# Performance work log

Hardware: AMD Instinct MI355X
Metric: run time of the kernel (lower is better)

## Reference

```python
import jax, jax.numpy as jnp
import numpy as np

GAMMA_LL = 1.7595e11            # gyromagnetic ratio (rad/s/T), class constant
MU0 = np.float32(4e-7 * np.pi)  # vacuum permeability
A_EXCH = 3.65e-12               # exchange stiffness (J/m)
ALPHA = 0.01                    # Gilbert damping (run)
ALPHA_RELAX = 0.5               # high damping used by relax()
DT = 5e-12                      # timestep (s)
DX = DY = 50e-9                 # cell size (m)
NX = NY = 256
T = 1024
RELAX_STEPS = 100               # relax_timesteps class constant


def _laplacian(m):
    # m: (1,3,NX,NY); 5-point Laplacian with Neumann (replicate) boundaries
    mp = jnp.pad(m, ((0, 0), (0, 0), (1, 1), (1, 1)), mode="edge")
    lap_x = (mp[:, :, 2:, 1:-1] + mp[:, :, :-2, 1:-1] - 2.0 * m) / (DX * DX)
    lap_y = (mp[:, :, 1:-1, 2:] + mp[:, :, 1:-1, :-2] - 2.0 * m) / (DY * DY)
    return lap_x + lap_y


def _B_eff(m, B_ext, Msat):
    # B_ext + exchange + (local thin-film) demag
    B_exch = (2.0 * A_EXCH / Msat) * _laplacian(m)
    zhat = jnp.array([0.0, 0.0, 1.0], m.dtype).reshape(1, 3, 1, 1)
    B_demag = -MU0 * Msat * m * zhat
    return B_ext + B_exch + B_demag


def _torque_LLG(m, B_ext, Msat, alpha):
    m_x_B = jnp.cross(m, _B_eff(m, B_ext, Msat), axis=1)
    return -(m_x_B + alpha * jnp.cross(m, m_x_B, axis=1)) / (1.0 + alpha * alpha)


def _rk4_step(m, B_ext, Msat, alpha):
    h = GAMMA_LL * DT
    k1 = _torque_LLG(m, B_ext, Msat, alpha)
    k2 = _torque_LLG(m + 0.5 * h * k1, B_ext, Msat, alpha)
    k3 = _torque_LLG(m + 0.5 * h * k2, B_ext, Msat, alpha)
    k4 = _torque_LLG(m + h * k3, B_ext, Msat, alpha)
    return m + (h / 6.0) * (k1 + 2.0 * k2 + 2.0 * k3 + k4)


def setup_inputs() -> dict:
    key = jax.random.key(0)
    signal = jax.random.normal(key, (1, T, 1), jnp.float32)
    # 60 mT out-of-plane bias field
    B_ext = jnp.zeros((1, 3, NX, NY), jnp.float32).at[:, 2].set(0.06)
    Msat = 1.4e5 * jnp.ones((1, 1, NX, NY), jnp.float32)
    # source antenna: 1 mT/unit signal on Bx in a 20x20 patch
    src_mask = jnp.zeros((1, 3, NX, NY), jnp.float32).at[:, 0, 20:40, 118:138].set(1e-3)
    probe_mask = jnp.zeros((NX, NY), jnp.float32).at[216:236, 118:138].set(1.0)
    return {"signal": signal, "B_ext": B_ext, "Msat": Msat,
            "src_mask": src_mask, "probe_mask": probe_mask}


def reference(signal, B_ext, Msat, src_mask, probe_mask):
    dtype = signal.dtype
    m_init = jnp.zeros((1, 3, NX, NY), dtype).at[:, 2].set(1.0)

    # relax(): high-damping RK4 steps under no_grad
    B_ext_c = jax.lax.stop_gradient(B_ext)
    Msat_c = jax.lax.stop_gradient(Msat)
    m0 = jax.lax.fori_loop(
        0, RELAX_STEPS,
        lambda i, m: _rk4_step(m, B_ext_c, Msat_c, ALPHA_RELAX),
        m_init)
    m0 = jax.lax.stop_gradient(m0)

    pm_sum = jnp.sum(probe_mask)

    def step(m, s):
        Bt = B_ext + s * src_mask            # inject_sources
        m = _rk4_step(m, Bt, Msat, ALPHA)    # rk4_step_LLG
        # measure_probes: mean mx of (m - m0) * Msat over probe region
        out = jnp.sum(((m - m0) * Msat)[:, 0] * probe_mask) / pm_sum
        return m, out

    m_final, outs = jax.lax.scan(jax.checkpoint(step), m0, signal[0, :, 0])
    return outs[None, :]  # (1, T) concatenated probe outputs
```

## Files before the change

### kernel.cpp

```cpp
#include <hip/hip_runtime.h>

#define TST   1024
#define OWN   16
#define HALO  4
#define TDIM  24
#define NT    576
#define NB    256

typedef float v4f __attribute__((ext_vector_type(4)));

#define AG __HIP_MEMORY_SCOPE_AGENT
__device__ __forceinline__ float agload (const float* p){ return __hip_atomic_load (p, __ATOMIC_RELAXED, AG); }
__device__ __forceinline__ int   agloadi(const int* p)  { return __hip_atomic_load (p, __ATOMIC_RELAXED, AG); }
__device__ __forceinline__ void  agstoref(float* p,float v){      __hip_atomic_store(p, v, __ATOMIC_RELAXED, AG); }
__device__ __forceinline__ void  agstorei(int* p,int v) {         __hip_atomic_store(p, v, __ATOMIC_RELAXED, AG); }

__device__ __forceinline__ v4f ld16_dev(const v4f* p) {
    v4f r;
    asm volatile("global_load_dwordx4 %0, %1, off sc1\n\ts_waitcnt vmcnt(0)"
                 : "=v"(r) : "v"(p) : "memory");
    return r;
}
__device__ __forceinline__ void st16_dev(v4f* p, v4f v) {
    asm volatile("global_store_dwordx4 %0, %1, off sc1" :: "v"(p), "v"(v) : "memory");
}

__global__ void __launch_bounds__(NT)
mm_solver(const float* __restrict__ signal,
          const float* __restrict__ B_ext,
          const float* __restrict__ Msat,
          const float* __restrict__ src_mask,
          const float* __restrict__ probe_mask,
          float* __restrict__ out,
          float* __restrict__ ws)
{
    const int b  = (int)blockIdx.x;
    const int bx = b & 15, by = b >> 4;
    const int t  = (int)threadIdx.x;
    const int tr = t / TDIM, tc = t % TDIM;

    const int grow = by * OWN - HALO + tr;
    const int gcol = bx * OWN - HALO + tc;
    const bool inG = (grow >= 0 && grow < 256 && gcol >= 0 && gcol < 256);
    const bool own = (tr >= HALO && tr < HALO + OWN && tc >= HALO && tc < HALO + OWN);

    v4f*   pub   = (v4f*)ws;
    float* priv  = ws + 2 * NB * 256 * 4;
    int*   doneA = (int*)(priv + NB * TST);
    const int pubStride = NB * 256;

    __shared__ v4f  EB[2][TDIM * TDIM];
    __shared__ float sigS[TST];
    __shared__ int   hasP;
    __shared__ int   pfl[NB];
    __shared__ float redS[16];
    __shared__ float pmsS;

    const float invd   = (float)(1.0 / (double)((float)(50e-9 * 50e-9)));
    const float h      = (float)(1.7595e11 * 5e-12);
    const float hh     = (float)(0.5 * (1.7595e11 * 5e-12));
    const float h6     = (float)((1.7595e11 * 5e-12) / 6.0);
    const float alpha  = 0.01f;
    const float inv1a2 = (float)(1.0 / (1.0 + 0.01 * 0.01));

    const int growc = grow < 0 ? 0 : (grow > 255 ? 255 : grow);
    const int gcolc = gcol < 0 ? 0 : (gcol > 255 ? 255 : gcol);
    const int idxg  = growc * 256 + gcolc;
    const float bxv = B_ext[idxg], byv = B_ext[65536 + idxg], bzv = B_ext[131072 + idxg];
    const float ms  = Msat[idxg];
    const float sxv = src_mask[idxg], syv = src_mask[65536 + idxg], szv = src_mask[131072 + idxg];
    const float pm  = probe_mask[idxg];
    const float ce   = 7.3e-12f / ms;
    const float cdem = -(float)(4.0e-7 * 3.14159265358979323846) * ms;

    const int idx  = t;
    const int offU = ((tr < TDIM - 1) && (grow < 255)) ?  TDIM : 0;
    const int offD = ((tr > 0)        && (grow > 0))   ? -TDIM : 0;
    const int offR = ((tc < TDIM - 1) && (gcol < 255)) ?  1 : 0;
    const int offL = ((tc > 0)        && (gcol > 0))   ? -1 : 0;

    const int ownerB  = ((grow >> 4) << 4) | (gcol >> 4);
    const int ownerCi = ((grow & 15) << 4) | (gcol & 15);
    const int slotOff = ownerB * 256 + ownerCi;

    float mx = 0.0f, my = 0.0f, mz = 1.0f;

    if (own) st16_dev(pub + slotOff, (v4f){0.0f, 0.0f, 1.0f, __int_as_float(0)});
    for (int k = t; k < TST; k += NT) sigS[k] = signal[k];
    if (t == 0) hasP = 0;
    __syncthreads();
    const bool pcell = own && (pm != 0.0f);
    if (pcell) atomicOr(&hasP, 1);
    const bool waveP = (__ballot(pcell) != 0ull);
    __syncthreads();
    const int hasPr = hasP;
    if (hasPr) for (int k = t; k < TST; k += NT) agstoref(&priv[b * TST + k], 0.0f);

    const bool haloT = inG && !own;
    float ex, ey, ez, ax, ay, az, kx, ky, kz, btx, bty, btz;

#define STAGE(SB) do { \
    const v4f u = EB[SB][idx + offU]; \
    const v4f d = EB[SB][idx + offD]; \
    const v4f r = EB[SB][idx + offR]; \
    const v4f l = EB[SB][idx + offL]; \
    float lx = ((u.x + d.x - 2.0f * ex) + (r.x + l.x - 2.0f * ex)) * invd; \
    float ly = ((u.y + d.y - 2.0f * ey) + (r.y + l.y - 2.0f * ey)) * invd; \
    float lz = ((u.z + d.z - 2.0f * ez) + (r.z + l.z - 2.0f * ez)) * invd; \
    float Bx = btx + ce * lx; \
    float By = bty + ce * ly; \
    float Bz = btz + ce * lz + cdem * ez; \
    float cx = ey * Bz - ez * By; \
    float cy = ez * Bx - ex * Bz; \
    float cz = ex * By - ey * Bx; \
    float dx = ey * cz - ez * cy; \
    float dy = ez * cx - ex * cz; \
    float dz = ex * cy - ey * cx; \
    kx = -(cx + alpha * dx) * inv1a2; \
    ky = -(cy + alpha * dy) * inv1a2; \
    kz = -(cz + alpha * dz) * inv1a2; \
} while (0)

#define WRE(DB) do { EB[DB][idx] = (v4f){ex, ey, ez, 0.0f}; } while (0)

    for (int i = 0; i < TST; ++i) {
        const float s = sigS[i];

        if (haloT) {
            const v4f* p = pub + (i & 1) * pubStride + slotOff;
            for (;;) {
                v4f hv = ld16_dev(p);
                if (__float_as_int(hv.w) >= i) { mx = hv.x; my = hv.y; mz = hv.z; break; }
                __builtin_amdgcn_s_sleep(1);
            }
        }

        btx = bxv + s * sxv;  bty = byv + s * syv;  btz = bzv + s * szv;
        ex = mx; ey = my; ez = mz;
        WRE(0);
        __syncthreads();

        STAGE(0);
        ax = kx; ay = ky; az = kz;
        ex = mx + hh * kx; ey = my + hh * ky; ez = mz + hh * kz;
        WRE(1);
        __syncthreads();

        STAGE(1);
        ax += 2.0f * kx; ay += 2.0f * ky; az += 2.0f * kz;
        ex = mx + hh * kx; ey = my + hh * ky; ez = mz + hh * kz;
        WRE(0);
        __syncthreads();

        STAGE(0);
        ax += 2.0f * kx; ay += 2.0f * ky; az += 2.0f * kz;
        ex = mx + h * kx; ey = my + h * ky; ez = mz + h * kz;
        WRE(1);
        __syncthreads();

        STAGE(1);
        ax += kx; ay += ky; az += kz;
        mx += h6 * ax; my += h6 * ay; mz += h6 * az;

        if (own) st16_dev(pub + ((i + 1) & 1) * pubStride + slotOff,
                          (v4f){mx, my, mz, __int_as_float(i + 1)});

        if (waveP) {
            float c = pcell ? mx * ms * pm : 0.0f;
            #pragma unroll
            for (int off = 32; off > 0; off >>= 1) c += __shfl_down(c, off, 64);
            if ((t & 63) == 0) atomicAdd(&priv[b * TST + i], c);
        }
    }

    __syncthreads();
    if (t == 0) agstorei(&doneA[b], 0x5D0000 | hasPr);

    if (b == 0) {
        if (t < NB) {
            int v;
            for (;;) { v = agloadi(&doneA[t]); if ((v & ~1) == 0x5D0000) break;
                       __builtin_amdgcn_s_sleep(8); }
            pfl[t] = v & 1;
        }
        __syncthreads();
        float ps = 0.0f;
        for (int k = t; k < 65536; k += NT) ps += probe_mask[k];
        #pragma unroll
        for (int off = 32; off > 0; off >>= 1) ps += __shfl_down(ps, off, 64);
        if ((t & 63) == 0) redS[t >> 6] = ps;
        __syncthreads();
        if (t == 0) { float q = 0.0f; for (int w = 0; w < 9; ++w) q += redS[w]; pmsS = q; }
        __syncthreads();
        const float pms = pmsS;
        for (int o = t; o < TST; o += NT) {
            float sm = 0.0f;
            for (int j = 0; j < NB; ++j) if (pfl[j]) sm += agload(&priv[j * TST + o]);
            out[o] = sm / pms;
        }
    }
}

extern "C" void kernel_launch(void* const* d_in, const int* in_sizes, int n_in,
                              void* d_out, int out_size, void* d_ws, size_t ws_size,
                              hipStream_t stream)
{
    const float* signal = (const float*)d_in[0];
    const float* B_ext  = (const float*)d_in[1];
    const float* Msat   = (const float*)d_in[2];
    const float* src    = (const float*)d_in[3];
    const float* probe  = (const float*)d_in[4];
    float* out = (float*)d_out;
    float* ws  = (float*)d_ws;

    void* args[] = { &signal, &B_ext, &Msat, &src, &probe, &out, &ws };
    (void)in_sizes; (void)n_in; (void)out_size; (void)ws_size;

    hipLaunchCooperativeKernel(reinterpret_cast<void*>(mm_solver),
                               dim3(NB), dim3(NT), args, 0, stream);
}
```

Baseline: 3.217 ms.

## Replace block barriers with per-wave neighbor counters in LDS

Each of the four `__syncthreads` per RK4 step is replaced by point-to-point sync. Every wave publishes a stage counter in shared memory and spins only until its two adjacent waves have reached the same stage, which the 5-point stencil needs. The s_sleep in the halo polling loop is also removed. The global exchange buffer is re-indexed in plain row-major cell order instead of owner-block order. The intent is to cut barrier latency and wakeup delay, at the cost of busy-spinning on LDS and relying on subtle ordering (WAR hazards between the double buffers) for correctness.

New measurement: 2.985 ms. 1.08x faster.

```diff
diff --git a/kernel.cpp b/kernel.cpp
--- a/kernel.cpp
+++ b/kernel.cpp
@@ -38,6 +38,7 @@
     const int bx = b & 15, by = b >> 4;
     const int t  = (int)threadIdx.x;
     const int tr = t / TDIM, tc = t % TDIM;
+    const int wv = t >> 6;
 
     const int grow = by * OWN - HALO + tr;
     const int gcol = bx * OWN - HALO + tc;
@@ -45,16 +46,33 @@
     const bool own = (tr >= HALO && tr < HALO + OWN && tc >= HALO && tc < HALO + OWN);
 
     v4f*   pub   = (v4f*)ws;
-    float* priv  = ws + 2 * NB * 256 * 4;
+    float* priv  = ws + 2 * 65536 * 4;
     int*   doneA = (int*)(priv + NB * TST);
-    const int pubStride = NB * 256;
+    const int pubStride = 65536;
 
     __shared__ v4f  EB[2][TDIM * TDIM];
     __shared__ float sigS[TST];
+    __shared__ int  wctr[11];
     __shared__ int   hasP;
     __shared__ int   pfl[NB];
     __shared__ float redS[16];
     __shared__ float pmsS;
+
+    volatile int* cl  = (volatile int*)&wctr[wv];
+    volatile int* cr  = (volatile int*)&wctr[wv + 2];
+    volatile int* cme = (volatile int*)&wctr[wv + 1];
+    const bool lane0 = ((t & 63) == 0);
+
+#define PUB_CTR(G) do { \
+    asm volatile("s_waitcnt lgkmcnt(0)" ::: "memory"); \
+    if (lane0) *cme = (G); \
+    asm volatile("" ::: "memory"); \
+} while (0)
+#define SPIN_NBR(G) do { \
+    while (*cl < (G)) {} \
+    while (*cr < (G)) {} \
+    asm volatile("" ::: "memory"); \
+} while (0)
 
     const float invd   = (float)(1.0 / (double)((float)(50e-9 * 50e-9)));
     const float h      = (float)(1.7595e11 * 5e-12);
@@ -79,15 +97,14 @@
     const int offR = ((tc < TDIM - 1) && (gcol < 255)) ?  1 : 0;
     const int offL = ((tc > 0)        && (gcol > 0))   ? -1 : 0;
 
-    const int ownerB  = ((grow >> 4) << 4) | (gcol >> 4);
-    const int ownerCi = ((grow & 15) << 4) | (gcol & 15);
-    const int slotOff = ownerB * 256 + ownerCi;
+    const int slotOff = idxg;
 
     float mx = 0.0f, my = 0.0f, mz = 1.0f;
 
     if (own) st16_dev(pub + slotOff, (v4f){0.0f, 0.0f, 1.0f, __int_as_float(0)});
     for (int k = t; k < TST; k += NT) sigS[k] = signal[k];
-    if (t == 0) hasP = 0;
+    if (t < 11) wctr[t] = (t == 0 || t == 10) ? 0x7fffffff : -1;
+    if (t == 11) hasP = 0;
     __syncthreads();
     const bool pcell = own && (pm != 0.0f);
     if (pcell) atomicOr(&hasP, 1);
@@ -95,6 +112,7 @@
     __syncthreads();
     const int hasPr = hasP;
     if (hasPr) for (int k = t; k < TST; k += NT) agstoref(&priv[b * TST + k], 0.0f);
+    __syncthreads();
 
     const bool haloT = inG && !own;
     float ex, ey, ez, ax, ay, az, kx, ky, kz, btx, bty, btz;
@@ -125,39 +143,42 @@
 
     for (int i = 0; i < TST; ++i) {
         const float s = sigS[i];
+        const int  g0 = i << 2;
 
         if (haloT) {
             const v4f* p = pub + (i & 1) * pubStride + slotOff;
             for (;;) {
                 v4f hv = ld16_dev(p);
                 if (__float_as_int(hv.w) >= i) { mx = hv.x; my = hv.y; mz = hv.z; break; }
-                __builtin_amdgcn_s_sleep(1);
             }
         }
 
         btx = bxv + s * sxv;  bty = byv + s * syv;  btz = bzv + s * szv;
         ex = mx; ey = my; ez = mz;
         WRE(0);
-        __syncthreads();
-
+        PUB_CTR(g0);
+        SPIN_NBR(g0);
         STAGE(0);
         ax = kx; ay = ky; az = kz;
         ex = mx + hh * kx; ey = my + hh * ky; ez = mz + hh * kz;
         WRE(1);
-        __syncthreads();
-
+        PUB_CTR(g0 + 1);
+
+        SPIN_NBR(g0 + 1);
         STAGE(1);
         ax += 2.0f * kx; ay += 2.0f * ky; az += 2.0f * kz;
         ex = mx + hh * kx; ey = my + hh * ky; ez = mz + hh * kz;
         WRE(0);
-        __syncthreads();
-
+        PUB_CTR(g0 + 2);
+
+        SPIN_NBR(g0 + 2);
         STAGE(0);
         ax += 2.0f * kx; ay += 2.0f * ky; az += 2.0f * kz;
         ex = mx + h * kx; ey = my + h * ky; ez = mz + h * kz;
         WRE(1);
-        __syncthreads();
-
+        PUB_CTR(g0 + 3);
+
+        SPIN_NBR(g0 + 3);
         STAGE(1);
         ax += kx; ay += ky; az += kz;
         mx += h6 * ax; my += h6 * ay; mz += h6 * az;
@@ -169,7 +190,7 @@
             float c = pcell ? mx * ms * pm : 0.0f;
             #pragma unroll
             for (int off = 32; off > 0; off >>= 1) c += __shfl_down(c, off, 64);
-            if ((t & 63) == 0) atomicAdd(&priv[b * TST + i], c);
+            if (lane0) atomicAdd(&priv[b * TST + i], c);
         }
     }
 
@@ -188,7 +209,7 @@
         for (int k = t; k < 65536; k += NT) ps += probe_mask[k];
         #pragma unroll
         for (int off = 32; off > 0; off >>= 1) ps += __shfl_down(ps, off, 64);
-        if ((t & 63) == 0) redS[t >> 6] = ps;
+        if (lane0) redS[wv] = ps;
         __syncthreads();
         if (t == 0) { float q = 0.0f; for (int w = 0; w < 9; ++w) q += redS[w]; pmsS = q; }
         __syncthreads();
```
